# Kernel tuning notes

Hardware: AMD Instinct MI355X
Metric: run time of the kernel (lower is better)

## Reference

```python
import jax, jax.numpy as jnp
import numpy as np

N, H = 16, 200
EMB, H1, H2 = 64, 128, 64
NUM_SKILLS = 2000
D_USER, D_ITEM, D_LANG = 100, 100, 10
TIME_BINS = np.array([1, 3600, 24 * 3600, 7 * 24 * 3600], dtype=np.float32)
NUM_TIME_CATS = TIME_BINS.size + 2  # 6

# strictly-lower-triangular pair indices, row-major: pair (i, j) with j < i
PAIR_I, PAIR_J = np.tril_indices(H, k=-1)          # skill_indices, history_indices_selected
P = PAIR_I.size                                    # adjusted_history_len = H*(H-1)/2
ar = np.arange(H)
SUM_IDX = np.concatenate([ar * (ar - 1) // 2, [H * (H - 1) // 2]]).astype(np.int64)  # len H+1


def setup_inputs() -> dict:
    key = jax.random.key(0)
    ks = jax.random.split(key, 16)
    users = jax.random.normal(ks[0], (N, D_USER), jnp.float32)
    items = jax.random.normal(ks[1], (N * H, D_ITEM), jnp.float32)
    langs = jax.random.normal(ks[2], (N * H, D_LANG), jnp.float32)
    skills = jax.random.randint(ks[3], (N, H), 0, NUM_SKILLS)
    timestamps = jnp.sort(jax.random.uniform(ks[4], (N, H), jnp.float32) * 2e6, axis=1)
    targets = (jax.random.uniform(ks[5], (N, H)) > 0.5).astype(jnp.float32)
    mask = jnp.ones((N * H,), dtype=bool)
    emb_table = jax.random.normal(ks[6], (NUM_SKILLS, EMB), jnp.float32) * 0.1
    emb_table = emb_table.at[0].set(0.0)  # padding_idx=0
    W1 = jax.random.normal(ks[7], (H1, 2 * EMB + NUM_TIME_CATS), jnp.float32) * 0.05
    b1 = jnp.zeros((H1,), jnp.float32)
    W2 = jax.random.normal(ks[8], (H2, H1), jnp.float32) * 0.05
    b2 = jnp.zeros((H2,), jnp.float32)
    W3 = jax.random.normal(ks[9], (1, H2), jnp.float32) * 0.05
    b3 = jnp.zeros((1,), jnp.float32)
    num_features = D_USER + D_ITEM + D_LANG + NUM_SKILLS
    linW = jax.random.normal(ks[10], (1, num_features + 2 * NUM_SKILLS), jnp.float32) * 0.01
    linb = jnp.zeros((1,), jnp.float32)
    return {"users": users, "items": items, "langs": langs, "skills": skills,
            "timestamps": timestamps, "targets": targets, "mask": mask,
            "emb_table": emb_table, "W1": W1, "b1": b1, "W2": W2, "b2": b2,
            "W3": W3, "b3": b3, "linW": linW, "linb": linb}


def _forward(users, items, langs, skills, timestamps, targets, mask,
             emb_table, W1, b1, W2, b2, W3, b3, linW, linb):
    bins = jnp.asarray(TIME_BINS)
    pi = jnp.asarray(PAIR_I)
    pj = jnp.asarray(PAIR_J)
    # gather pair embeddings: [N*P, EMB]
    emb = emb_table[skills]                       # [N, H, EMB]
    e_i = emb[:, pi].reshape(-1, EMB)             # skill at position i
    e_j = emb[:, pj].reshape(-1, EMB)             # history skill j < i
    # time-delta categories
    dt = (timestamps[:, pi] - timestamps[:, pj]).reshape(-1)
    cats = jnp.sum(dt[:, None] > bins[None, :], axis=1) + 1
    pad = skills == 0
    pad_pair = pad[:, pi].reshape(-1) | pad[:, pj].reshape(-1)
    cats = jnp.where(pad_pair, 0, cats)
    dt_oh = jax.nn.one_hot(cats, NUM_TIME_CATS, dtype=jnp.float32)
    # pairwise similarity MLP -> tanh scalar, [N, P]
    x = jnp.concatenate([e_i, e_j, dt_oh], axis=1)
    h = jax.nn.relu(x @ W1.T + b1)
    h = jax.nn.relu(h @ W2.T + b2)
    sim = jnp.tanh(h @ W3.T + b3).reshape(N, P)

    sum_idx = jnp.asarray(SUM_IDX)

    def seg_sum(v):  # cumsum-based segment sum over pairs grouped by i -> [N, H]
        cs = jnp.concatenate([jnp.zeros((N, 1), v.dtype), jnp.cumsum(v, axis=1)], axis=1)
        return cs[:, sum_idx[1:]] - cs[:, sum_idx[:-1]]

    flat_skills = skills.reshape(-1)              # [N*H]
    padf = (flat_skills != 0).astype(jnp.float32)
    rows = jnp.arange(N * H)
    v_total = seg_sum(sim).reshape(-1) * padf
    v_correct = seg_sum(sim * targets[:, pi]).reshape(-1) * padf
    tcf = jnp.zeros((N * H, 2 * NUM_SKILLS), jnp.float32)
    tcf = tcf.at[rows, flat_skills].set(v_total)
    tcf = tcf.at[rows, flat_skills + NUM_SKILLS].set(v_correct)

    feats = jnp.concatenate([
        jnp.repeat(users, H, axis=0), items, langs,
        jax.nn.one_hot(flat_skills, NUM_SKILLS, dtype=jnp.float32), tcf], axis=1)
    logits = feats @ linW.T + linb                # [N*H, 1]
    preds = logits.reshape(-1)
    labels = targets.reshape(-1)
    maskf = mask.astype(jnp.float32)
    # BCEWithLogits (reduction='none') + z-term, z_weight=0.0; mask applied as weight
    bce = jnp.logaddexp(0.0, preds) - preds * labels
    eps = 1e-6
    yc = jnp.clip(labels, eps, 1.0 - eps)
    z = jnp.log(yc / (1.0 - yc))
    z_weight = 0.0
    loss = (bce + z_weight * jnp.square(z - preds)) * maskf
    return loss, jax.nn.sigmoid(preds), labels


def reference(users, items, langs, skills, timestamps, targets, mask,
              emb_table, W1, b1, W2, b2, W3, b3, linW, linb):
    return _forward(users, items, langs, skills, timestamps, targets, mask,
                    emb_table, W1, b1, W2, b2, W3, b3, linW, linb)
```

## Files before the change

### kernel.cpp

```cpp
#include <hip/hip_runtime.h>
#include <math.h>

#define N_B     16
#define H_LEN   200
#define NH      3200
#define EMB     64
#define HID1    128
#define HID2    64
#define NCAT    6
#define W1_COLS 134

#define TI 16
#define NTILE_I 13
#define NTRI (NTILE_I * (NTILE_I + 1) / 2)
#define PAIRS_PER_BLK 7
#define NSLICE 13

#define WS_VT   0
#define WS_W2F  51200
#define WS_W1F  55296
#define WS_CF   63488

typedef __attribute__((ext_vector_type(8))) __bf16 bf16x8;
typedef __attribute__((ext_vector_type(8))) unsigned short ushort8;
typedef __attribute__((ext_vector_type(4))) float f32x4;

__device__ __forceinline__ unsigned short bfbits(float x) {
    return __builtin_bit_cast(unsigned short, (__bf16)x);
}

__global__ void k0_setup(const float* __restrict__ W1,
                         const float* __restrict__ b1,
                         const float* __restrict__ W2,
                         float* __restrict__ ws) {
    int idx = blockIdx.x * 256 + threadIdx.x;
    if (idx < 16384) {
        int e = idx & 7, l = (idx >> 3) & 63, ks = (idx >> 9) & 1;
        int nt = (idx >> 10) & 7, h = idx >> 13;
        int col = l & 15, quad = l >> 4;
        int c = nt * 16 + col;
        int kg = h * EMB + ks * 32 + quad * 8 + e;
        ((unsigned short*)(ws + WS_W1F))[idx] = bfbits(W1[c * W1_COLS + kg]);
        return;
    }
    idx -= 16384;
    if (idx < 8192) {
        int e = idx & 7, lane = (idx >> 3) & 63, f = idx >> 9;
        int mt = f >> 2, kk = f & 3, col = lane & 15, quad = lane >> 4;
        float w = W2[(mt * 16 + col) * HID1 + (kk * 4 + quad) * 8 + e];
        ((unsigned short*)(ws + WS_W2F))[idx] = bfbits(w);
        return;
    }
    idx -= 8192;
    if (idx < NCAT * HID1) {
        int c = idx >> 7, u = idx & 127;
        ws[WS_CF + idx] = W1[u * W1_COLS + 2 * EMB + c] + b1[u];
    }
}

__global__ __launch_bounds__(512, 2)
void k2_mfma(const int* __restrict__ skills,
             const float* __restrict__ ts,
             const float* __restrict__ emb,
             const float* __restrict__ b2,
             const float* __restrict__ W3,
             const float* __restrict__ b3,
             float* __restrict__ ws) {
    __shared__ float esmI[TI][68];
    __shared__ float esmJ[TI][68];
    __shared__ float Asm[TI][132];
    __shared__ float Bsm[TI][132];
    __shared__ float Csm[NCAT][132];
    __shared__ float tsiS[TI], tsjS[TI];
    __shared__ int   skiS[TI], skjS[TI];

    int t = threadIdx.x, lane = t & 63, w = t >> 6;
    int col = lane & 15, quad = lane >> 4;

    int bid = blockIdx.x;
    int n = bid & 15;
    int s = bid >> 4;
    int base = n * H_LEN;
    int tt = s * PAIRS_PER_BLK;
    int ti = (int)((sqrtf(8.f * (float)tt + 1.f) - 1.f) * 0.5f);
    while (ti * (ti + 1) / 2 > tt) --ti;
    while ((ti + 1) * (ti + 2) / 2 <= tt) ++ti;
    int tj = tt - ti * (ti + 1) / 2;

    if (t < 192) {
        int cr = t >> 5, cc = t & 31;
        *(f32x4*)&Csm[cr][cc * 4] = *(const f32x4*)(ws + WS_CF + cr * HID1 + cc * 4);
    }
    int half = w >> 2, ntq = (w & 3) * 2;
    const ushort8* w1f = (const ushort8*)(ws + WS_W1F);
    bf16x8 w1frag[2][2];
    #pragma unroll
    for (int l = 0; l < 2; ++l)
        #pragma unroll
        for (int ks = 0; ks < 2; ++ks)
            w1frag[l][ks] = __builtin_bit_cast(bf16x8,
                w1f[((half * 8 + ntq + l) * 2 + ks) * 64 + lane]);
    const ushort8* w2f = (const ushort8*)(ws + WS_W2F);
    bf16x8 afr[4][4];
    #pragma unroll
    for (int mt = 0; mt < 4; ++mt)
        #pragma unroll
        for (int kk = 0; kk < 4; ++kk)
            afr[mt][kk] = __builtin_bit_cast(bf16x8, w2f[(mt * 4 + kk) * 64 + lane]);
    f32x4 b2acc[4], w3f4[4];
    #pragma unroll
    for (int mt = 0; mt < 4; ++mt)
        #pragma unroll
        for (int r = 0; r < 4; ++r) {
            int u = mt * 16 + quad * 4 + r;
            b2acc[mt][r] = b2[u];
            w3f4[mt][r]  = W3[u];
        }
    float b3s = b3[0];

    int side = t >> 8, rr = (t >> 4) & 15, c4 = t & 15;
    {
        int g = min((side ? tj : ti) * TI + rr, H_LEN - 1);
        int sk = skills[base + g];
        f32x4 v = *(const f32x4*)(emb + (size_t)sk * EMB + c4 * 4);
        if (side) *(f32x4*)&esmJ[rr][c4 * 4] = v;
        else      *(f32x4*)&esmI[rr][c4 * 4] = v;
    }
    if (t < 32) {
        int sd = t >> 4, r2 = t & 15;
        int g = min((sd ? tj : ti) * TI + r2, H_LEN - 1);
        float tv = ts[base + g]; int sv = skills[base + g];
        if (sd) { tsjS[r2] = tv; skjS[r2] = sv; }
        else    { tsiS[r2] = tv; skiS[r2] = sv; }
    }
    __syncthreads();

    for (int it = 0; it < PAIRS_PER_BLK; ++it) {
        bool diag = (ti == tj);
        int i0 = ti * TI, j0 = tj * TI;

        {
            float (*es)[68]  = half ? esmJ : esmI;
            float (*zs)[132] = half ? Bsm : Asm;
            f32x4 acc0 = {0.f,0.f,0.f,0.f}, acc1 = {0.f,0.f,0.f,0.f};
            #pragma unroll
            for (int ks = 0; ks < 2; ++ks) {
                f32x4 a0 = *(const f32x4*)&es[col][ks * 32 + quad * 8];
                f32x4 a1 = *(const f32x4*)&es[col][ks * 32 + quad * 8 + 4];
                bf16x8 af;
                #pragma unroll
                for (int e = 0; e < 4; ++e) { af[e] = (__bf16)a0[e]; af[4 + e] = (__bf16)a1[e]; }
                acc0 = __builtin_amdgcn_mfma_f32_16x16x32_bf16(af, w1frag[0][ks], acc0, 0, 0, 0);
                acc1 = __builtin_amdgcn_mfma_f32_16x16x32_bf16(af, w1frag[1][ks], acc1, 0, 0, 0);
            }
            #pragma unroll
            for (int r = 0; r < 4; ++r) {
                zs[quad * 4 + r][(ntq + 0) * 16 + col] = acc0[r];
                zs[quad * 4 + r][(ntq + 1) * 16 + col] = acc1[r];
            }
        }

        int nti = ti, ntj = tj + 1;
        if (ntj > nti) { ++nti; ntj = 0; }
        bool hasNext = (it + 1 < PAIRS_PER_BLK);
        f32x4 pref = {0.f,0.f,0.f,0.f};
        float ptv = 0.f; int psv = 0;
        if (hasNext) {
            int g = min((side ? ntj : nti) * TI + rr, H_LEN - 1);
            int sk = skills[base + g];
            pref = *(const f32x4*)(emb + (size_t)sk * EMB + c4 * 4);
            if (t < 32) {
                int sd = t >> 4, r2 = t & 15;
                int g2 = min((sd ? ntj : nti) * TI + r2, H_LEN - 1);
                ptv = ts[base + g2]; psv = skills[base + g2];
            }
        }
        int sj = skjS[col]; float tsjv = tsjS[col];
        int   siA[2]; float tsiA[2];
        #pragma unroll
        for (int ss = 0; ss < 2; ++ss) { siA[ss] = skiS[w * 2 + ss]; tsiA[ss] = tsiS[w * 2 + ss]; }

        __syncthreads();

        if (hasNext) {
            if (side) *(f32x4*)&esmJ[rr][c4 * 4] = pref;
            else      *(f32x4*)&esmI[rr][c4 * 4] = pref;
            if (t < 32) {
                int sd = t >> 4, r2 = t & 15;
                if (sd) { tsjS[r2] = ptv; skjS[r2] = psv; }
                else    { tsiS[r2] = ptv; skiS[r2] = psv; }
            }
        }

        f32x4 braw[8];
        #pragma unroll
        for (int kk = 0; kk < 4; ++kk) {
            braw[2 * kk]     = *(const f32x4*)&Bsm[col][kk * 32 + quad * 8];
            braw[2 * kk + 1] = *(const f32x4*)&Bsm[col][kk * 32 + quad * 8 + 4];
        }

        #pragma unroll
        for (int ss = 0; ss < 2; ++ss) {
            int ii = w * 2 + ss;
            int gi = i0 + ii;
            if (gi >= H_LEN) continue;
            if (diag && ii == 0) continue;

            int si = siA[ss]; float tsiv = tsiA[ss];
            float dtv = tsiv - tsjv;
            int cat = (si == 0 || sj == 0) ? 0
                    : 1 + (dtv > 1.f) + (dtv > 3600.f) + (dtv > 86400.f) + (dtv > 604800.f);

            f32x4 acc[4];
            #pragma unroll
            for (int kk = 0; kk < 4; ++kk) {
                f32x4 a0 = *(const f32x4*)&Asm[ii][kk * 32 + quad * 8];
                f32x4 a1 = *(const f32x4*)&Asm[ii][kk * 32 + quad * 8 + 4];
                f32x4 c0 = *(const f32x4*)&Csm[cat][kk * 32 + quad * 8];
                f32x4 c1 = *(const f32x4*)&Csm[cat][kk * 32 + quad * 8 + 4];
                f32x4 t0 = a0 + braw[2 * kk] + c0;
                f32x4 t1 = a1 + braw[2 * kk + 1] + c1;
                t0 = __builtin_elementwise_max(t0, (f32x4)0.f);
                t1 = __builtin_elementwise_max(t1, (f32x4)0.f);
                bf16x8 v;
                #pragma unroll
                for (int e = 0; e < 4; ++e) { v[e] = (__bf16)t0[e]; v[4 + e] = (__bf16)t1[e]; }
                #pragma unroll
                for (int mt = 0; mt < 4; ++mt)
                    acc[mt] = __builtin_amdgcn_mfma_f32_16x16x32_bf16(
                        afr[mt][kk], v, kk == 0 ? b2acc[mt] : acc[mt], 0, 0, 0);
            }

            f32x4 ps = {0.f, 0.f, 0.f, 0.f};
            #pragma unroll
            for (int mt = 0; mt < 4; ++mt) {
                f32x4 hp = __builtin_elementwise_max(acc[mt], (f32x4)0.f);
                ps = hp * w3f4[mt] + ps;
            }
            float partial = (ps[0] + ps[1]) + (ps[2] + ps[3]);
            partial += __shfl_xor(partial, 16);
            partial += __shfl_xor(partial, 32);
            float xc = fminf(fmaxf(partial + b3s, -15.f), 15.f);
            float e2 = __expf(2.f * xc);
            float sim = (e2 - 1.f) / (e2 + 1.f);

            int gj = j0 + col;
            bool valid = (gj < gi);
            sim = valid ? sim : 0.f;
            sim += __shfl_xor(sim, 1);
            sim += __shfl_xor(sim, 2);
            sim += __shfl_xor(sim, 4);
            sim += __shfl_xor(sim, 8);
            if (lane == 0) ws[WS_VT + (size_t)(base + gi) * 16 + tj] = sim;
        }

        __syncthreads();
        ti = nti; tj = ntj;
    }
}

__global__ __launch_bounds__(256)
void k3_final(const float* __restrict__ users,
              const float* __restrict__ items,
              const float* __restrict__ langs,
              const int* __restrict__ skills,
              const float* __restrict__ targets,
              const float* __restrict__ linW,
              const float* __restrict__ linb,
              const float* __restrict__ ws,
              float* __restrict__ out) {
    int r = blockIdx.x * 4 + (threadIdx.x >> 6);
    int lane = threadIdx.x & 63;
    int n = r / H_LEN;
    int gi = r - n * H_LEN;
    float acc = 0.f;
    for (int idx = lane; idx < 210; idx += 64) {
        float f;
        if (idx < 100)      f = users[n * 100 + idx];
        else if (idx < 200) f = items[r * 100 + (idx - 100)];
        else                f = langs[r * 10 + (idx - 200)];
        acc = fmaf(f, linW[idx], acc);
    }
    #pragma unroll
    for (int off = 32; off > 0; off >>= 1) acc += __shfl_xor(acc, off);

    int cnt = (gi >> 4) + ((gi & 15) ? 1 : 0);
    float v = (lane < cnt) ? ws[WS_VT + (size_t)r * 16 + lane] : 0.f;
    v += __shfl_xor(v, 1);
    v += __shfl_xor(v, 2);
    v += __shfl_xor(v, 4);
    v += __shfl_xor(v, 8);

    if (lane == 0) {
        int s = skills[r];
        float tgt = targets[r];
        float vtv = v;
        if (s == 0) vtv = 0.f;
        float vcv = vtv * tgt;
        float logit = acc + linW[210 + s] + vtv * linW[2210 + s]
                    + vcv * linW[4210 + s] + linb[0];
        float sp = logit > 0.f ? logit + log1pf(expf(-logit)) : log1pf(expf(logit));
        float loss = sp - logit * tgt;
        float sig = 1.f / (1.f + expf(-logit));
        out[r]          = loss;
        out[NH + r]     = sig;
        out[2 * NH + r] = tgt;
    }
}

extern "C" void kernel_launch(void* const* d_in, const int* in_sizes, int n_in,
                              void* d_out, int out_size, void* d_ws, size_t ws_size,
                              hipStream_t stream) {
    const float* users   = (const float*)d_in[0];
    const float* items   = (const float*)d_in[1];
    const float* langs   = (const float*)d_in[2];
    const int*   skills  = (const int*)d_in[3];
    const float* ts      = (const float*)d_in[4];
    const float* targets = (const float*)d_in[5];
    const float* emb     = (const float*)d_in[7];
    const float* W1      = (const float*)d_in[8];
    const float* b1      = (const float*)d_in[9];
    const float* W2      = (const float*)d_in[10];
    const float* b2      = (const float*)d_in[11];
    const float* W3      = (const float*)d_in[12];
    const float* b3      = (const float*)d_in[13];
    const float* linW    = (const float*)d_in[14];
    const float* linb    = (const float*)d_in[15];
    float* ws  = (float*)d_ws;
    float* out = (float*)d_out;

    hipLaunchKernelGGL(k0_setup, dim3(99), dim3(256), 0, stream, W1, b1, W2, ws);
    hipLaunchKernelGGL(k2_mfma, dim3(N_B * NSLICE), dim3(512), 0, stream,
                       skills, ts, emb, b2, W3, b3, ws);
    hipLaunchKernelGGL(k3_final, dim3(NH / 4), dim3(256), 0, stream,
                       users, items, langs, skills, targets, linW, linb, ws, out);
}
```

Before: 114.2 us.

## Fuse setup, pair-MLP and final kernels into one cooperative launch

```diff
diff --git a/kernel.cpp b/kernel.cpp
--- a/kernel.cpp
+++ b/kernel.cpp
@@ -1,5 +1,8 @@
 #include <hip/hip_runtime.h>
+#include <hip/hip_cooperative_groups.h>
 #include <math.h>
+
+namespace cg = cooperative_groups;
 
 #define N_B     16
 #define H_LEN   200
@@ -12,9 +15,9 @@
 
 #define TI 16
 #define NTILE_I 13
-#define NTRI (NTILE_I * (NTILE_I + 1) / 2)
 #define PAIRS_PER_BLK 7
 #define NSLICE 13
+#define NBLK   (N_B * NSLICE)
 
 #define WS_VT   0
 #define WS_W2F  51200
@@ -29,43 +32,24 @@
     return __builtin_bit_cast(unsigned short, (__bf16)x);
 }
 
-__global__ void k0_setup(const float* __restrict__ W1,
-                         const float* __restrict__ b1,
-                         const float* __restrict__ W2,
-                         float* __restrict__ ws) {
-    int idx = blockIdx.x * 256 + threadIdx.x;
-    if (idx < 16384) {
-        int e = idx & 7, l = (idx >> 3) & 63, ks = (idx >> 9) & 1;
-        int nt = (idx >> 10) & 7, h = idx >> 13;
-        int col = l & 15, quad = l >> 4;
-        int c = nt * 16 + col;
-        int kg = h * EMB + ks * 32 + quad * 8 + e;
-        ((unsigned short*)(ws + WS_W1F))[idx] = bfbits(W1[c * W1_COLS + kg]);
-        return;
-    }
-    idx -= 16384;
-    if (idx < 8192) {
-        int e = idx & 7, lane = (idx >> 3) & 63, f = idx >> 9;
-        int mt = f >> 2, kk = f & 3, col = lane & 15, quad = lane >> 4;
-        float w = W2[(mt * 16 + col) * HID1 + (kk * 4 + quad) * 8 + e];
-        ((unsigned short*)(ws + WS_W2F))[idx] = bfbits(w);
-        return;
-    }
-    idx -= 8192;
-    if (idx < NCAT * HID1) {
-        int c = idx >> 7, u = idx & 127;
-        ws[WS_CF + idx] = W1[u * W1_COLS + 2 * EMB + c] + b1[u];
-    }
-}
-
 __global__ __launch_bounds__(512, 2)
-void k2_mfma(const int* __restrict__ skills,
+void k_fused(const int* __restrict__ skills,
              const float* __restrict__ ts,
              const float* __restrict__ emb,
+             const float* __restrict__ W1,
+             const float* __restrict__ b1,
+             const float* __restrict__ W2,
              const float* __restrict__ b2,
              const float* __restrict__ W3,
              const float* __restrict__ b3,
-             float* __restrict__ ws) {
+             const float* __restrict__ users,
+             const float* __restrict__ items,
+             const float* __restrict__ langs,
+             const float* __restrict__ targets,
+             const float* __restrict__ linW,
+             const float* __restrict__ linb,
+             float* __restrict__ ws,
+             float* __restrict__ out) {
     __shared__ float esmI[TI][68];
     __shared__ float esmJ[TI][68];
     __shared__ float Asm[TI][132];
@@ -76,235 +60,255 @@
 
     int t = threadIdx.x, lane = t & 63, w = t >> 6;
     int col = lane & 15, quad = lane >> 4;
-
     int bid = blockIdx.x;
-    int n = bid & 15;
-    int s = bid >> 4;
-    int base = n * H_LEN;
-    int tt = s * PAIRS_PER_BLK;
-    int ti = (int)((sqrtf(8.f * (float)tt + 1.f) - 1.f) * 0.5f);
-    while (ti * (ti + 1) / 2 > tt) --ti;
-    while ((ti + 1) * (ti + 2) / 2 <= tt) ++ti;
-    int tj = tt - ti * (ti + 1) / 2;
-
-    if (t < 192) {
-        int cr = t >> 5, cc = t & 31;
-        *(f32x4*)&Csm[cr][cc * 4] = *(const f32x4*)(ws + WS_CF + cr * HID1 + cc * 4);
+
+    {
+        int idx = bid * 512 + t;
+        if (idx < 16384) {
+            int e = idx & 7, l = (idx >> 3) & 63, ks = (idx >> 9) & 1;
+            int nt = (idx >> 10) & 7, h = idx >> 13;
+            int c = nt * 16 + (l & 15);
+            int kg = h * EMB + ks * 32 + (l >> 4) * 8 + e;
+            ((unsigned short*)(ws + WS_W1F))[idx] = bfbits(W1[c * W1_COLS + kg]);
+        } else if (idx < 16384 + 8192) {
+            int j = idx - 16384;
+            int e = j & 7, ln = (j >> 3) & 63, f = j >> 9;
+            int mt = f >> 2, kk = f & 3;
+            float wv = W2[(mt * 16 + (ln & 15)) * HID1 + (kk * 4 + (ln >> 4)) * 8 + e];
+            ((unsigned short*)(ws + WS_W2F))[j] = bfbits(wv);
+        } else if (idx < 16384 + 8192 + NCAT * HID1) {
+            int j = idx - 16384 - 8192;
+            int c = j >> 7, u = j & 127;
+            ws[WS_CF + j] = W1[u * W1_COLS + 2 * EMB + c] + b1[u];
+        }
     }
-    int half = w >> 2, ntq = (w & 3) * 2;
-    const ushort8* w1f = (const ushort8*)(ws + WS_W1F);
-    bf16x8 w1frag[2][2];
-    #pragma unroll
-    for (int l = 0; l < 2; ++l)
+    __threadfence();
+    cg::this_grid().sync();
+
+    {
+        int n = bid & 15;
+        int s = bid >> 4;
+        int base = n * H_LEN;
+        int tt = s * PAIRS_PER_BLK;
+        int ti = (int)((sqrtf(8.f * (float)tt + 1.f) - 1.f) * 0.5f);
+        while (ti * (ti + 1) / 2 > tt) --ti;
+        while ((ti + 1) * (ti + 2) / 2 <= tt) ++ti;
+        int tj = tt - ti * (ti + 1) / 2;
+
+        if (t < 192) {
+            int cr = t >> 5, cc = t & 31;
+            *(f32x4*)&Csm[cr][cc * 4] = *(const f32x4*)(ws + WS_CF + cr * HID1 + cc * 4);
+        }
+        int half = w >> 2, ntq = (w & 3) * 2;
+        const ushort8* w1f = (const ushort8*)(ws + WS_W1F);
+        bf16x8 w1frag[2][2];
         #pragma unroll
-        for (int ks = 0; ks < 2; ++ks)
-            w1frag[l][ks] = __builtin_bit_cast(bf16x8,
-                w1f[((half * 8 + ntq + l) * 2 + ks) * 64 + lane]);
-    const ushort8* w2f = (const ushort8*)(ws + WS_W2F);
-    bf16x8 afr[4][4];
-    #pragma unroll
-    for (int mt = 0; mt < 4; ++mt)
+        for (int l = 0; l < 2; ++l)
+            #pragma unroll
+            for (int ks = 0; ks < 2; ++ks)
+                w1frag[l][ks] = __builtin_bit_cast(bf16x8,
+                    w1f[((half * 8 + ntq + l) * 2 + ks) * 64 + lane]);
+        const ushort8* w2f = (const ushort8*)(ws + WS_W2F);
+        bf16x8 afr[4][4];
         #pragma unroll
-        for (int kk = 0; kk < 4; ++kk)
-            afr[mt][kk] = __builtin_bit_cast(bf16x8, w2f[(mt * 4 + kk) * 64 + lane]);
-    f32x4 b2acc[4], w3f4[4];
-    #pragma unroll
-    for (int mt = 0; mt < 4; ++mt)
+        for (int mt = 0; mt < 4; ++mt)
+            #pragma unroll
+            for (int kk = 0; kk < 4; ++kk)
+                afr[mt][kk] = __builtin_bit_cast(bf16x8, w2f[(mt * 4 + kk) * 64 + lane]);
+        f32x4 b2acc[4], w3f4[4];
         #pragma unroll
-        for (int r = 0; r < 4; ++r) {
-            int u = mt * 16 + quad * 4 + r;
-            b2acc[mt][r] = b2[u];
-            w3f4[mt][r]  = W3[u];
-        }
-    float b3s = b3[0];
-
-    int side = t >> 8, rr = (t >> 4) & 15, c4 = t & 15;
-    {
-        int g = min((side ? tj : ti) * TI + rr, H_LEN - 1);
-        int sk = skills[base + g];
-        f32x4 v = *(const f32x4*)(emb + (size_t)sk * EMB + c4 * 4);
-        if (side) *(f32x4*)&esmJ[rr][c4 * 4] = v;
-        else      *(f32x4*)&esmI[rr][c4 * 4] = v;
+        for (int mt = 0; mt < 4; ++mt)
+            #pragma unroll
+            for (int r = 0; r < 4; ++r) {
+                int u = mt * 16 + quad * 4 + r;
+                b2acc[mt][r] = b2[u];
+                w3f4[mt][r]  = W3[u];
+            }
+        float b3s = b3[0];
+
+        int side = t >> 8, rr = (t >> 4) & 15, c4 = t & 15;
+        {
+            int g = min((side ? tj : ti) * TI + rr, H_LEN - 1);
+            int sk = skills[base + g];
+            f32x4 v = *(const f32x4*)(emb + (size_t)sk * EMB + c4 * 4);
+            if (side) *(f32x4*)&esmJ[rr][c4 * 4] = v;
+            else      *(f32x4*)&esmI[rr][c4 * 4] = v;
+        }
+        if (t < 32) {
+            int sd = t >> 4, r2 = t & 15;
+            int g = min((sd ? tj : ti) * TI + r2, H_LEN - 1);
+            float tv = ts[base + g]; int sv = skills[base + g];
+            if (sd) { tsjS[r2] = tv; skjS[r2] = sv; }
+            else    { tsiS[r2] = tv; skiS[r2] = sv; }
+        }
+        __syncthreads();
+
+        for (int it = 0; it < PAIRS_PER_BLK; ++it) {
+            bool diag = (ti == tj);
+            int i0 = ti * TI, j0 = tj * TI;
+
+            {
+                float (*es)[68]  = half ? esmJ : esmI;
+                float (*zs)[132] = half ? Bsm : Asm;
+                f32x4 acc0 = {0.f,0.f,0.f,0.f}, acc1 = {0.f,0.f,0.f,0.f};
+                #pragma unroll
+                for (int ks = 0; ks < 2; ++ks) {
+                    f32x4 a0 = *(const f32x4*)&es[col][ks * 32 + quad * 8];
+                    f32x4 a1 = *(const f32x4*)&es[col][ks * 32 + quad * 8 + 4];
+                    bf16x8 af;
+                    #pragma unroll
+                    for (int e = 0; e < 4; ++e) { af[e] = (__bf16)a0[e]; af[4 + e] = (__bf16)a1[e]; }
+                    acc0 = __builtin_amdgcn_mfma_f32_16x16x32_bf16(af, w1frag[0][ks], acc0, 0, 0, 0);
+                    acc1 = __builtin_amdgcn_mfma_f32_16x16x32_bf16(af, w1frag[1][ks], acc1, 0, 0, 0);
+                }
+                #pragma unroll
+                for (int r = 0; r < 4; ++r) {
+                    zs[quad * 4 + r][(ntq + 0) * 16 + col] = acc0[r];
+                    zs[quad * 4 + r][(ntq + 1) * 16 + col] = acc1[r];
+                }
+            }
+
+            int nti = ti, ntj = tj + 1;
+            if (ntj > nti) { ++nti; ntj = 0; }
+            bool hasNext = (it + 1 < PAIRS_PER_BLK);
+            f32x4 pref = {0.f,0.f,0.f,0.f};
+            float ptv = 0.f; int psv = 0;
+            if (hasNext) {
+                int g = min((side ? ntj : nti) * TI + rr, H_LEN - 1);
+                int sk = skills[base + g];
+                pref = *(const f32x4*)(emb + (size_t)sk * EMB + c4 * 4);
+                if (t < 32) {
+                    int sd = t >> 4, r2 = t & 15;
+                    int g2 = min((sd ? ntj : nti) * TI + r2, H_LEN - 1);
+                    ptv = ts[base + g2]; psv = skills[base + g2];
+                }
+            }
+            int sj = skjS[col]; float tsjv = tsjS[col];
+            int   siA[2]; float tsiA[2];
+            #pragma unroll
+            for (int ss = 0; ss < 2; ++ss) { siA[ss] = skiS[w * 2 + ss]; tsiA[ss] = tsiS[w * 2 + ss]; }
+
+            __syncthreads();
+
+            if (hasNext) {
+                if (side) *(f32x4*)&esmJ[rr][c4 * 4] = pref;
+                else      *(f32x4*)&esmI[rr][c4 * 4] = pref;
+                if (t < 32) {
+                    int sd = t >> 4, r2 = t & 15;
+                    if (sd) { tsjS[r2] = ptv; skjS[r2] = psv; }
+                    else    { tsiS[r2] = ptv; skiS[r2] = psv; }
+                }
+            }
+
+            f32x4 braw[8];
+            #pragma unroll
+            for (int kk = 0; kk < 4; ++kk) {
+                braw[2 * kk]     = *(const f32x4*)&Bsm[col][kk * 32 + quad * 8];
+                braw[2 * kk + 1] = *(const f32x4*)&Bsm[col][kk * 32 + quad * 8 + 4];
+            }
+
+            #pragma unroll
+            for (int ss = 0; ss < 2; ++ss) {
+                int ii = w * 2 + ss;
+                int gi = i0 + ii;
+                if (gi >= H_LEN) continue;
+                if (diag && ii == 0) continue;
+
+                int si = siA[ss]; float tsiv = tsiA[ss];
+                float dtv = tsiv - tsjv;
+                int cat = (si == 0 || sj == 0) ? 0
+                        : 1 + (dtv > 1.f) + (dtv > 3600.f) + (dtv > 86400.f) + (dtv > 604800.f);
+
+                f32x4 acc[4];
+                #pragma unroll
+                for (int kk = 0; kk < 4; ++kk) {
+                    f32x4 a0 = *(const f32x4*)&Asm[ii][kk * 32 + quad * 8];
+                    f32x4 a1 = *(const f32x4*)&Asm[ii][kk * 32 + quad * 8 + 4];
+                    f32x4 c0 = *(const f32x4*)&Csm[cat][kk * 32 + quad * 8];
+                    f32x4 c1 = *(const f32x4*)&Csm[cat][kk * 32 + quad * 8 + 4];
+                    f32x4 t0 = a0 + braw[2 * kk] + c0;
+                    f32x4 t1 = a1 + braw[2 * kk + 1] + c1;
+                    t0 = __builtin_elementwise_max(t0, (f32x4)0.f);
+                    t1 = __builtin_elementwise_max(t1, (f32x4)0.f);
+                    bf16x8 v;
+                    #pragma unroll
+                    for (int e = 0; e < 4; ++e) { v[e] = (__bf16)t0[e]; v[4 + e] = (__bf16)t1[e]; }
+                    #pragma unroll
+                    for (int mt = 0; mt < 4; ++mt)
+                        acc[mt] = __builtin_amdgcn_mfma_f32_16x16x32_bf16(
+                            afr[mt][kk], v, kk == 0 ? b2acc[mt] : acc[mt], 0, 0, 0);
+                }
+
+                f32x4 ps = {0.f, 0.f, 0.f, 0.f};
+                #pragma unroll
+                for (int mt = 0; mt < 4; ++mt) {
+                    f32x4 hp = __builtin_elementwise_max(acc[mt], (f32x4)0.f);
+                    ps = hp * w3f4[mt] + ps;
+                }
+                float partial = (ps[0] + ps[1]) + (ps[2] + ps[3]);
+                partial += __shfl_xor(partial, 16);
+                partial += __shfl_xor(partial, 32);
+                float xc = fminf(fmaxf(partial + b3s, -15.f), 15.f);
+                float e2 = __expf(2.f * xc);
+                float sim = (e2 - 1.f) / (e2 + 1.f);
+
+                int gj = j0 + col;
+                bool valid = (gj < gi);
+                sim = valid ? sim : 0.f;
+                sim += __shfl_xor(sim, 1);
+                sim += __shfl_xor(sim, 2);
+                sim += __shfl_xor(sim, 4);
+                sim += __shfl_xor(sim, 8);
+                if (lane == 0) ws[WS_VT + (size_t)(base + gi) * 16 + tj] = sim;
+            }
+
+            __syncthreads();
+            ti = nti; tj = ntj;
+        }
     }
-    if (t < 32) {
-        int sd = t >> 4, r2 = t & 15;
-        int g = min((sd ? tj : ti) * TI + r2, H_LEN - 1);
-        float tv = ts[base + g]; int sv = skills[base + g];
-        if (sd) { tsjS[r2] = tv; skjS[r2] = sv; }
-        else    { tsiS[r2] = tv; skiS[r2] = sv; }
-    }
-    __syncthreads();
-
-    for (int it = 0; it < PAIRS_PER_BLK; ++it) {
-        bool diag = (ti == tj);
-        int i0 = ti * TI, j0 = tj * TI;
-
-        {
-            float (*es)[68]  = half ? esmJ : esmI;
-            float (*zs)[132] = half ? Bsm : Asm;
-            f32x4 acc0 = {0.f,0.f,0.f,0.f}, acc1 = {0.f,0.f,0.f,0.f};
-            #pragma unroll
-            for (int ks = 0; ks < 2; ++ks) {
-                f32x4 a0 = *(const f32x4*)&es[col][ks * 32 + quad * 8];
-                f32x4 a1 = *(const f32x4*)&es[col][ks * 32 + quad * 8 + 4];
-                bf16x8 af;
-                #pragma unroll
-                for (int e = 0; e < 4; ++e) { af[e] = (__bf16)a0[e]; af[4 + e] = (__bf16)a1[e]; }
-                acc0 = __builtin_amdgcn_mfma_f32_16x16x32_bf16(af, w1frag[0][ks], acc0, 0, 0, 0);
-                acc1 = __builtin_amdgcn_mfma_f32_16x16x32_bf16(af, w1frag[1][ks], acc1, 0, 0, 0);
-            }
-            #pragma unroll
-            for (int r = 0; r < 4; ++r) {
-                zs[quad * 4 + r][(ntq + 0) * 16 + col] = acc0[r];
-                zs[quad * 4 + r][(ntq + 1) * 16 + col] = acc1[r];
-            }
-        }
-
-        int nti = ti, ntj = tj + 1;
-        if (ntj > nti) { ++nti; ntj = 0; }
-        bool hasNext = (it + 1 < PAIRS_PER_BLK);
-        f32x4 pref = {0.f,0.f,0.f,0.f};
-        float ptv = 0.f; int psv = 0;
-        if (hasNext) {
-            int g = min((side ? ntj : nti) * TI + rr, H_LEN - 1);
-            int sk = skills[base + g];
-            pref = *(const f32x4*)(emb + (size_t)sk * EMB + c4 * 4);
-            if (t < 32) {
-                int sd = t >> 4, r2 = t & 15;
-                int g2 = min((sd ? ntj : nti) * TI + r2, H_LEN - 1);
-                ptv = ts[base + g2]; psv = skills[base + g2];
-            }
-        }
-        int sj = skjS[col]; float tsjv = tsjS[col];
-        int   siA[2]; float tsiA[2];
+    __threadfence();
+    cg::this_grid().sync();
+
+    if (bid < 200) {
         #pragma unroll
-        for (int ss = 0; ss < 2; ++ss) { siA[ss] = skiS[w * 2 + ss]; tsiA[ss] = tsiS[w * 2 + ss]; }
-
-        __syncthreads();
-
-        if (hasNext) {
-            if (side) *(f32x4*)&esmJ[rr][c4 * 4] = pref;
-            else      *(f32x4*)&esmI[rr][c4 * 4] = pref;
-            if (t < 32) {
-                int sd = t >> 4, r2 = t & 15;
-                if (sd) { tsjS[r2] = ptv; skjS[r2] = psv; }
-                else    { tsiS[r2] = ptv; skiS[r2] = psv; }
-            }
-        }
-
-        f32x4 braw[8];
-        #pragma unroll
-        for (int kk = 0; kk < 4; ++kk) {
-            braw[2 * kk]     = *(const f32x4*)&Bsm[col][kk * 32 + quad * 8];
-            braw[2 * kk + 1] = *(const f32x4*)&Bsm[col][kk * 32 + quad * 8 + 4];
-        }
-
-        #pragma unroll
-        for (int ss = 0; ss < 2; ++ss) {
-            int ii = w * 2 + ss;
-            int gi = i0 + ii;
-            if (gi >= H_LEN) continue;
-            if (diag && ii == 0) continue;
-
-            int si = siA[ss]; float tsiv = tsiA[ss];
-            float dtv = tsiv - tsjv;
-            int cat = (si == 0 || sj == 0) ? 0
-                    : 1 + (dtv > 1.f) + (dtv > 3600.f) + (dtv > 86400.f) + (dtv > 604800.f);
-
-            f32x4 acc[4];
-            #pragma unroll
-            for (int kk = 0; kk < 4; ++kk) {
-                f32x4 a0 = *(const f32x4*)&Asm[ii][kk * 32 + quad * 8];
-                f32x4 a1 = *(const f32x4*)&Asm[ii][kk * 32 + quad * 8 + 4];
-                f32x4 c0 = *(const f32x4*)&Csm[cat][kk * 32 + quad * 8];
-                f32x4 c1 = *(const f32x4*)&Csm[cat][kk * 32 + quad * 8 + 4];
-                f32x4 t0 = a0 + braw[2 * kk] + c0;
-                f32x4 t1 = a1 + braw[2 * kk + 1] + c1;
-                t0 = __builtin_elementwise_max(t0, (f32x4)0.f);
-                t1 = __builtin_elementwise_max(t1, (f32x4)0.f);
-                bf16x8 v;
-                #pragma unroll
-                for (int e = 0; e < 4; ++e) { v[e] = (__bf16)t0[e]; v[4 + e] = (__bf16)t1[e]; }
-                #pragma unroll
-                for (int mt = 0; mt < 4; ++mt)
-                    acc[mt] = __builtin_amdgcn_mfma_f32_16x16x32_bf16(
-                        afr[mt][kk], v, kk == 0 ? b2acc[mt] : acc[mt], 0, 0, 0);
-            }
-
-            f32x4 ps = {0.f, 0.f, 0.f, 0.f};
-            #pragma unroll
-            for (int mt = 0; mt < 4; ++mt) {
-                f32x4 hp = __builtin_elementwise_max(acc[mt], (f32x4)0.f);
-                ps = hp * w3f4[mt] + ps;
-            }
-            float partial = (ps[0] + ps[1]) + (ps[2] + ps[3]);
-            partial += __shfl_xor(partial, 16);
-            partial += __shfl_xor(partial, 32);
-            float xc = fminf(fmaxf(partial + b3s, -15.f), 15.f);
-            float e2 = __expf(2.f * xc);
-            float sim = (e2 - 1.f) / (e2 + 1.f);
-
-            int gj = j0 + col;
-            bool valid = (gj < gi);
-            sim = valid ? sim : 0.f;
-            sim += __shfl_xor(sim, 1);
-            sim += __shfl_xor(sim, 2);
-            sim += __shfl_xor(sim, 4);
-            sim += __shfl_xor(sim, 8);
-            if (lane == 0) ws[WS_VT + (size_t)(base + gi) * 16 + tj] = sim;
-        }
-
-        __syncthreads();
-        ti = nti; tj = ntj;
-    }
-}
-
-__global__ __launch_bounds__(256)
-void k3_final(const float* __restrict__ users,
-              const float* __restrict__ items,
-              const float* __restrict__ langs,
-              const int* __restrict__ skills,
-              const float* __restrict__ targets,
-              const float* __restrict__ linW,
-              const float* __restrict__ linb,
-              const float* __restrict__ ws,
-              float* __restrict__ out) {
-    int r = blockIdx.x * 4 + (threadIdx.x >> 6);
-    int lane = threadIdx.x & 63;
-    int n = r / H_LEN;
-    int gi = r - n * H_LEN;
-    float acc = 0.f;
-    for (int idx = lane; idx < 210; idx += 64) {
-        float f;
-        if (idx < 100)      f = users[n * 100 + idx];
-        else if (idx < 200) f = items[r * 100 + (idx - 100)];
-        else                f = langs[r * 10 + (idx - 200)];
-        acc = fmaf(f, linW[idx], acc);
-    }
-    #pragma unroll
-    for (int off = 32; off > 0; off >>= 1) acc += __shfl_xor(acc, off);
-
-    int cnt = (gi >> 4) + ((gi & 15) ? 1 : 0);
-    float v = (lane < cnt) ? ws[WS_VT + (size_t)r * 16 + lane] : 0.f;
-    v += __shfl_xor(v, 1);
-    v += __shfl_xor(v, 2);
-    v += __shfl_xor(v, 4);
-    v += __shfl_xor(v, 8);
-
-    if (lane == 0) {
-        int s = skills[r];
-        float tgt = targets[r];
-        float vtv = v;
-        if (s == 0) vtv = 0.f;
-        float vcv = vtv * tgt;
-        float logit = acc + linW[210 + s] + vtv * linW[2210 + s]
-                    + vcv * linW[4210 + s] + linb[0];
-        float sp = logit > 0.f ? logit + log1pf(expf(-logit)) : log1pf(expf(logit));
-        float loss = sp - logit * tgt;
-        float sig = 1.f / (1.f + expf(-logit));
-        out[r]          = loss;
-        out[NH + r]     = sig;
-        out[2 * NH + r] = tgt;
+        for (int ss2 = 0; ss2 < 2; ++ss2) {
+            int r = bid * 16 + w * 2 + ss2;
+            int n = r / H_LEN;
+            int gi = r - n * H_LEN;
+            float acc = 0.f;
+            for (int idx = lane; idx < 210; idx += 64) {
+                float f;
+                if (idx < 100)      f = users[n * 100 + idx];
+                else if (idx < 200) f = items[r * 100 + (idx - 100)];
+                else                f = langs[r * 10 + (idx - 200)];
+                acc = fmaf(f, linW[idx], acc);
+            }
+            #pragma unroll
+            for (int off = 32; off > 0; off >>= 1) acc += __shfl_xor(acc, off);
+
+            int cnt = (gi >> 4) + ((gi & 15) ? 1 : 0);
+            float v = (lane < cnt) ? ws[WS_VT + (size_t)r * 16 + lane] : 0.f;
+            v += __shfl_xor(v, 1);
+            v += __shfl_xor(v, 2);
+            v += __shfl_xor(v, 4);
+            v += __shfl_xor(v, 8);
+
+            if (lane == 0) {
+                int s = skills[r];
+                float tgt = targets[r];
+                float vtv = v;
+                if (s == 0) vtv = 0.f;
+                float vcv = vtv * tgt;
+                float logit = acc + linW[210 + s] + vtv * linW[2210 + s]
+                            + vcv * linW[4210 + s] + linb[0];
+                float sp = logit > 0.f ? logit + log1pf(expf(-logit)) : log1pf(expf(logit));
+                float loss = sp - logit * tgt;
+                float sig = 1.f / (1.f + expf(-logit));
+                out[r]          = loss;
+                out[NH + r]     = sig;
+                out[2 * NH + r] = tgt;
+            }
+        }
     }
 }
 
@@ -329,9 +333,10 @@
     float* ws  = (float*)d_ws;
     float* out = (float*)d_out;
 
-    hipLaunchKernelGGL(k0_setup, dim3(99), dim3(256), 0, stream, W1, b1, W2, ws);
-    hipLaunchKernelGGL(k2_mfma, dim3(N_B * NSLICE), dim3(512), 0, stream,
-                       skills, ts, emb, b2, W3, b3, ws);
-    hipLaunchKernelGGL(k3_final, dim3(NH / 4), dim3(256), 0, stream,
-                       users, items, langs, skills, targets, linW, linb, ws, out);
+    void* args[] = { (void*)&skills, (void*)&ts, (void*)&emb, (void*)&W1,
+                     (void*)&b1, (void*)&W2, (void*)&b2, (void*)&W3, (void*)&b3,
+                     (void*)&users, (void*)&items, (void*)&langs, (void*)&targets,
+                     (void*)&linW, (void*)&linb, (void*)&ws, (void*)&out };
+    hipLaunchCooperativeKernel((const void*)k_fused, dim3(NBLK), dim3(512),
+                               args, 0, stream);
 }
```

After: 228.9 us. +100.4%, slower.
